# Optimization experiments

Measured on AMD Instinct MI355X. Metric: run time of the kernel, lower is better.

Reference implementation:

```python
import math
import jax, jax.numpy as jnp
import numpy as np

N_HEADS = 8
WINDOW = 4


def _get_relative_embeddings(emb, length, window):
    # emb: [1, 2*window+1, k_channels] -> [1, 2*length-1, k_channels]
    pad_length = max(length - (window + 1), 0)
    start = max(window + 1 - length, 0)
    if pad_length > 0:
        emb = jnp.pad(emb, ((0, 0), (pad_length, pad_length), (0, 0)))
    return emb[:, start:start + 2 * length - 1]


def _relative_position_to_absolute_position(x):
    # x: [b, h, l, 2l-1] -> [b, h, l, l] (skewing trick)
    b, h, l, _ = x.shape
    x = jnp.pad(x, ((0, 0), (0, 0), (0, 0), (0, 1)))
    x_flat = x.reshape(b, h, l * 2 * l)
    x_flat = jnp.pad(x_flat, ((0, 0), (0, 0), (0, l - 1)))
    return x_flat.reshape(b, h, l + 1, 2 * l - 1)[:, :, :l, l - 1:]


def _absolute_position_to_relative_position(x):
    # x: [b, h, l, l] -> [b, h, l, 2l-1]
    b, h, l, _ = x.shape
    x = jnp.pad(x, ((0, 0), (0, 0), (0, 0), (0, l - 1)))
    x_flat = x.reshape(b, h, l * l + l * (l - 1))
    x_flat = jnp.pad(x_flat, ((0, 0), (0, 0), (l, 0)))
    return x_flat.reshape(b, h, l, 2 * l)[:, :, :, 1:]


def setup_inputs() -> dict:
    key = jax.random.key(0)
    ks = jax.random.split(key, 12)
    b, t, d = 4, 1024, 512
    kc = d // N_HEADS
    s = 1.0 / math.sqrt(d)
    return {
        "x": jax.random.normal(ks[0], (b, t, d), jnp.float32),
        "c": jax.random.normal(ks[1], (b, t, d), jnp.float32),
        "wq": jax.random.normal(ks[2], (d, d), jnp.float32) * s,
        "bq": jnp.zeros((d,), jnp.float32),
        "wk": jax.random.normal(ks[3], (d, d), jnp.float32) * s,
        "bk": jnp.zeros((d,), jnp.float32),
        "wv": jax.random.normal(ks[4], (d, d), jnp.float32) * s,
        "bv": jnp.zeros((d,), jnp.float32),
        "wo": jax.random.normal(ks[5], (d, d), jnp.float32) * s,
        "bo": jnp.zeros((d,), jnp.float32),
        "emb_rel_k": jax.random.normal(ks[6], (1, 2 * WINDOW + 1, kc), jnp.float32) * kc ** -0.5,
        "emb_rel_v": jax.random.normal(ks[7], (1, 2 * WINDOW + 1, kc), jnp.float32) * kc ** -0.5,
    }


def reference(x, c, wq, bq, wk, bk, wv, bv, wo, bo, emb_rel_k, emb_rel_v):
    b, t, d = x.shape
    h = N_HEADS
    kc = d // h
    inv_sqrt = 1.0 / math.sqrt(kc)

    # 1x1 conv projections (pointwise matmul)
    q = x @ wq + bq   # [b, t, d]
    k = c @ wk + bk
    v = c @ wv + bv

    # Faithful reshape as in source: [b, t, d] -> [b, h, kc, t] -> [b, h, t, kc]
    q = q.reshape(b, h, kc, t).transpose(0, 1, 3, 2)
    k = k.reshape(b, h, kc, t).transpose(0, 1, 3, 2)
    v = v.reshape(b, h, kc, t).transpose(0, 1, 3, 2)

    scores = jnp.einsum('bhtd,bhsd->bhts', q, k) * inv_sqrt  # [b,h,t,t]

    # relative key logits
    key_rel = _get_relative_embeddings(emb_rel_k, t, WINDOW)[0]  # [2t-1, kc]
    rel_logits = jnp.einsum('bhtd,md->bhtm', q, key_rel)          # [b,h,t,2t-1]
    scores_local = _relative_position_to_absolute_position(rel_logits) * inv_sqrt
    scores = scores + scores_local

    p_attn = jax.nn.softmax(scores, axis=-1)
    output = jnp.einsum('bhts,bhsd->bhtd', p_attn, v)  # [b,h,t,kc]

    # relative value contribution
    rel_weights = _absolute_position_to_relative_position(p_attn)  # [b,h,t,2t-1]
    val_rel = _get_relative_embeddings(emb_rel_v, t, WINDOW)[0]    # [2t-1, kc]
    output = output + jnp.einsum('bhtm,md->bhtd', rel_weights, val_rel)

    # Faithful output reshape: [b,h,t,kc] -> [b,h,kc,t] -> [b,t,d]
    output = output.transpose(0, 1, 3, 2).reshape(b, t, d)
    out = output @ wo + bo
    return out
```

## Files before the change

### kernel.cpp

```cpp
#include <hip/hip_runtime.h>
#include <hip/hip_bf16.h>

#define NB 4
#define NT 1024
#define ND 512
#define NH 8
#define NKC 64

typedef __bf16 bf16x8 __attribute__((ext_vector_type(8)));
typedef float f32x4 __attribute__((ext_vector_type(4)));

__device__ __forceinline__ f32x4 MFMA(bf16x8 a, bf16x8 b, f32x4 c) {
    return __builtin_amdgcn_mfma_f32_16x16x32_bf16(a, b, c, 0, 0, 0);
}
__device__ __forceinline__ unsigned short f2bu(float v) {
    __hip_bfloat16 b = __float2bfloat16(v);
    return *(unsigned short*)&b;
}
__device__ __forceinline__ void split1(float v, unsigned short& h, unsigned short& l)
{
    __hip_bfloat16 hb = __float2bfloat16(v);
    float r = v - __bfloat162float(hb);
    __hip_bfloat16 lb = __float2bfloat16(r);
    h = *(unsigned short*)&hb;
    l = *(unsigned short*)&lb;
}
__device__ __forceinline__ void splitpack(const float4 a, const float4 b, uint4& h, uint4& l)
{
    union { unsigned short u[8]; uint4 v; } H, L;
    const float f[8] = {a.x, a.y, a.z, a.w, b.x, b.y, b.z, b.w};
    #pragma unroll
    for (int j = 0; j < 8; ++j) split1(f[j], H.u[j], L.u[j]);
    h = H.v; l = L.v;
}

__global__ __launch_bounds__(256)
void splitT_kernel(const float* __restrict__ w0, const float* __restrict__ w1,
                   const float* __restrict__ w2, const float* __restrict__ w3,
                   unsigned short* __restrict__ wT)
{
    __shared__ float tl[32][33];
    const float* w = (blockIdx.z == 0) ? w0 : (blockIdx.z == 1) ? w1
                   : (blockIdx.z == 2) ? w2 : w3;
    unsigned short* hi = wT + (size_t)blockIdx.z * 2 * (ND * ND);
    unsigned short* lo = hi + ND * ND;
    const int t = threadIdx.x;
    const int x0 = blockIdx.x * 32, y0 = blockIdx.y * 32;
    {
        const int r = t >> 3, c = (t & 7) * 4;
        const float4 v = *(const float4*)&w[(size_t)(y0 + r) * ND + x0 + c];
        tl[r][c] = v.x; tl[r][c+1] = v.y; tl[r][c+2] = v.z; tl[r][c+3] = v.w;
    }
    __syncthreads();
    {
        const int nr = t >> 3, k4 = (t & 7) * 4;
        unsigned short hh[4], ll[4];
        #pragma unroll
        for (int j = 0; j < 4; ++j) split1(tl[k4 + j][nr], hh[j], ll[j]);
        ushort4 h = make_ushort4(hh[0], hh[1], hh[2], hh[3]);
        ushort4 l = make_ushort4(ll[0], ll[1], ll[2], ll[3]);
        *(ushort4*)&hi[(size_t)(x0 + nr) * ND + y0 + k4] = h;
        *(ushort4*)&lo[(size_t)(x0 + nr) * ND + y0 + k4] = l;
    }
}

__global__ __launch_bounds__(256, 3)
void proj_mfma(const float* __restrict__ x, const float* __restrict__ cc,
               const unsigned short* __restrict__ wT,
               const float* __restrict__ bq, const float* __restrict__ bk,
               const float* __restrict__ bv,
               unsigned short* __restrict__ qh_o, unsigned short* __restrict__ ql_o,
               unsigned short* __restrict__ kh_o, unsigned short* __restrict__ vh_o)
{
    __shared__ unsigned short smem[12288];
    unsigned short* Ah = smem;
    unsigned short* Al = smem + 2048;
    unsigned short* Bh = smem + 4096;
    unsigned short* Bl = smem + 8192;
    unsigned short* Tr = smem;

    const int which = blockIdx.z;
    const float* A_g = (which == 0) ? x : cc;
    const unsigned short* Bh_g = wT + (size_t)which * 2 * (ND * ND);
    const unsigned short* Bl_g = Bh_g + ND * ND;
    const float* bias = (which == 0) ? bq : (which == 1) ? bk : bv;

    const int tid = threadIdx.x, l = tid & 63, w = tid >> 6;
    const int quad = l >> 4, lc = l & 15;
    const int wm = w & 1, wn = w >> 1;
    const int n0 = blockIdx.x * 128, m0 = blockIdx.y * 64;

    const int am = tid >> 2, ak = (tid & 3) * 8;
    const size_t aG = (size_t)(m0 + am) * ND + ak;
    const int bn = tid >> 1, bk2 = (tid & 1) * 16;
    const size_t bG = (size_t)(n0 + bn) * ND + bk2;

    float4 ra0 = *(const float4*)&A_g[aG];
    float4 ra1 = *(const float4*)&A_g[aG + 4];
    uint4 rb0 = *(const uint4*)&Bh_g[bG];
    uint4 rb1 = *(const uint4*)&Bh_g[bG + 8];
    uint4 rb2 = {}, rb3 = {};
    if (which != 2) {
        rb2 = *(const uint4*)&Bl_g[bG];
        rb3 = *(const uint4*)&Bl_g[bG + 8];
    }
    uint4 sh0, sl0;
    splitpack(ra0, ra1, sh0, sl0);

    f32x4 acc[2][4];
    #pragma unroll
    for (int mi = 0; mi < 2; ++mi)
        #pragma unroll
        for (int ni = 0; ni < 4; ++ni) acc[mi][ni] = (f32x4){0.f, 0.f, 0.f, 0.f};

    for (int k0 = 0; k0 < ND; k0 += 32) {
        __syncthreads();
        {
            *(uint4*)&Ah[am * 32 + ak] = sh0;
            *(uint4*)&Al[am * 32 + ak] = sl0;
            *(uint4*)&Bh[bn * 32 + bk2] = rb0; *(uint4*)&Bh[bn * 32 + bk2 + 8] = rb1;
            if (which != 2) {
                *(uint4*)&Bl[bn * 32 + bk2] = rb2; *(uint4*)&Bl[bn * 32 + bk2 + 8] = rb3;
            }
        }
        __syncthreads();
        const bool hasNext = (k0 + 32 < ND);
        if (hasNext) {
            const size_t aN = aG + k0 + 32, bN = bG + k0 + 32;
            ra0 = *(const float4*)&A_g[aN];
            ra1 = *(const float4*)&A_g[aN + 4];
            rb0 = *(const uint4*)&Bh_g[bN];
            rb1 = *(const uint4*)&Bh_g[bN + 8];
            if (which != 2) {
                rb2 = *(const uint4*)&Bl_g[bN];
                rb3 = *(const uint4*)&Bl_g[bN + 8];
            }
        }

        bf16x8 ah[2], al2[2], bh[4], bl[4];
        #pragma unroll
        for (int mi = 0; mi < 2; ++mi) {
            const int ar = (wm * 32 + mi * 16 + lc) * 32 + quad * 8;
            ah[mi] = *(const bf16x8*)&Ah[ar];
            al2[mi] = *(const bf16x8*)&Al[ar];
        }
        #pragma unroll
        for (int ni = 0; ni < 4; ++ni) {
            const int br = (wn * 64 + ni * 16 + lc) * 32 + quad * 8;
            bh[ni] = *(const bf16x8*)&Bh[br];
            if (which != 2) bl[ni] = *(const bf16x8*)&Bl[br];
        }
        if (which != 2) {
            #pragma unroll
            for (int mi = 0; mi < 2; ++mi)
                #pragma unroll
                for (int ni = 0; ni < 4; ++ni) {
                    acc[mi][ni] = MFMA(al2[mi], bh[ni], acc[mi][ni]);
                    acc[mi][ni] = MFMA(ah[mi], bl[ni], acc[mi][ni]);
                    acc[mi][ni] = MFMA(ah[mi], bh[ni], acc[mi][ni]);
                }
        } else {
            #pragma unroll
            for (int mi = 0; mi < 2; ++mi)
                #pragma unroll
                for (int ni = 0; ni < 4; ++ni) {
                    acc[mi][ni] = MFMA(al2[mi], bh[ni], acc[mi][ni]);
                    acc[mi][ni] = MFMA(ah[mi], bh[ni], acc[mi][ni]);
                }
        }
        if (hasNext) splitpack(ra0, ra1, sh0, sl0);
    }

    const int bb = m0 >> 10, tt0 = m0 & 1023;
    const int hh = tt0 >> 7, cch0 = (tt0 & 127) >> 1;
    const int bh_idx = bb * NH + hh;

    if (which == 2) {
        #pragma unroll
        for (int ni = 0; ni < 4; ++ni) {
            const int n = n0 + wn * 64 + ni * 16 + lc;
            const float bval = bias[n];
            #pragma unroll
            for (int mi = 0; mi < 2; ++mi)
                #pragma unroll
                for (int r = 0; r < 4; ++r) {
                    const int mloc = wm * 32 + mi * 16 + quad * 4 + r;
                    const int cch = cch0 + (mloc >> 1);
                    const int t = (mloc & 1) * 512 + n;
                    vh_o[(((size_t)bh_idx * 16 + (t >> 6)) * 64 + cch) * 64 + (t & 63)] =
                        f2bu(acc[mi][ni][r] + bval);
                }
        }
        return;
    }

    const int npass = (which == 0) ? 2 : 1;
    unsigned short* outp[2] = {(which == 0) ? qh_o : kh_o, ql_o};

    for (int pass = 0; pass < npass; ++pass) {
        __syncthreads();
        #pragma unroll
        for (int ni = 0; ni < 4; ++ni) {
            const int nloc = wn * 64 + ni * 16 + lc;
            const float bval = bias[n0 + nloc];
            #pragma unroll
            for (int mi = 0; mi < 2; ++mi)
                #pragma unroll
                for (int r = 0; r < 4; ++r) {
                    const int mloc = wm * 32 + mi * 16 + quad * 4 + r;
                    const float val = acc[mi][ni][r] + bval;
                    unsigned short hs, ls;
                    if (which == 0) { split1(val, hs, ls); }
                    else { hs = f2bu(val); ls = 0; }
                    Tr[((mloc & 1) * 128 + nloc) * 40 + (mloc >> 1)] =
                        (pass == 0) ? hs : ls;
                }
        }
        __syncthreads();
        {
            const int t = (tid >> 7) * 512 + n0 + (tid & 127);
            const size_t oa = ((size_t)bh_idx * NT + t) * NKC + cch0;
            const uint4 v0 = *(const uint4*)&Tr[tid * 40];
            const uint4 v1 = *(const uint4*)&Tr[tid * 40 + 8];
            const uint4 v2 = *(const uint4*)&Tr[tid * 40 + 16];
            const uint4 v3 = *(const uint4*)&Tr[tid * 40 + 24];
            *(uint4*)&outp[pass][oa]      = v0;
            *(uint4*)&outp[pass][oa + 8]  = v1;
            *(uint4*)&outp[pass][oa + 16] = v2;
            *(uint4*)&outp[pass][oa + 24] = v3;
        }
    }
}

__global__ __launch_bounds__(256, 4)
void attn_mfma(const unsigned short* __restrict__ qh_g, const unsigned short* __restrict__ ql_g,
               const unsigned short* __restrict__ kh_g,
               const unsigned short* __restrict__ vh_g,
               const float* __restrict__ embk, const float* __restrict__ embv,
               float* __restrict__ O0, float* __restrict__ O1,
               float* __restrict__ l0_g, float* __restrict__ l1_g)
{
    __shared__ unsigned short smem[19456];
    unsigned short* KsH = smem;
    unsigned short* Vt  = smem + 4608;
    unsigned short* Ps  = smem + 11264;
    float* bandv = (float*)(smem + 17920);
    unsigned short* EkH = smem + 11264;

    const int tid = threadIdx.x, l = tid & 63, w = tid >> 6;
    const int quad = l >> 4, lc = l & 15;
    const int q0 = (blockIdx.x >> 1) * 64;
    const int sh = blockIdx.x & 1;
    const int sBeg = sh * 512;
    const int hh = blockIdx.y, bb = blockIdx.z;
    const int bh = bb * NH + hh;
    const size_t qkBase = (size_t)bh * NT * NKC;
    const size_t vtBase = (size_t)bh * (16 * 64 * 64);
    float* Op = sh ? O1 : O0;
    float* lp = sh ? l1_g : l0_g;

    const int srow = tid >> 2, sseg = (tid & 3) * 16;

    auto loadKV = [&](uint4& k0r, uint4& k1r, uint4& v0r, uint4& v1r, int tile) {
        const size_t ka = qkBase + (size_t)(sBeg + tile * 64 + srow) * NKC + sseg;
        const size_t va = vtBase + (size_t)((sBeg >> 6) + tile) * 4096 + srow * 64 + sseg;
        k0r = *(const uint4*)&kh_g[ka];
        k1r = *(const uint4*)&kh_g[ka + 8];
        v0r = *(const uint4*)&vh_g[va];
        v1r = *(const uint4*)&vh_g[va + 8];
    };

    uint4 ak0, ak1, av0, av1, bk0, bk1, bv0, bv1;
    loadKV(ak0, ak1, av0, av1, 0);
    loadKV(bk0, bk1, bv0, bv1, 1);

    for (int idx = tid; idx < 16 * 72; idx += 256) {
        const int d = idx / 72, kc = idx - d * 72;
        EkH[idx] = f2bu((d < 9 && kc < 64) ? embk[d * 64 + kc] : 0.f);
    }
    for (int idx = tid; idx < 64 * 40; idx += 256) {
        const int c = idx / 40, col = 64 + (idx - c * 40);
        const int d = col - 64;
        Vt[c * 104 + col] = f2bu((d < 9) ? embv[d * 64 + c] : 0.f);
    }
    __syncthreads();

    bf16x8 qh[2], ql[2];
    {
        const int qg = q0 + w * 16 + lc;
        const size_t qa = qkBase + (size_t)qg * NKC + quad * 8;
        qh[0] = *(const bf16x8*)&qh_g[qa];
        qh[1] = *(const bf16x8*)&qh_g[qa + 32];
        ql[0] = *(const bf16x8*)&ql_g[qa];
        ql[1] = *(const bf16x8*)&ql_g[qa + 32];
    }

    {
        f32x4 accB = (f32x4){0.f, 0.f, 0.f, 0.f};
        #pragma unroll
        for (int kk = 0; kk < 2; ++kk) {
            const bf16x8 ebh = *(const bf16x8*)&EkH[lc * 72 + kk * 32 + quad * 8];
            accB = MFMA(ql[kk], ebh, accB);
            accB = MFMA(qh[kk], ebh, accB);
        }
        __syncthreads();
        if (lc <= 8) {
            #pragma unroll
            for (int r = 0; r < 4; ++r)
                bandv[(w * 16 + quad * 4 + r) * 12 + lc] = accB[r];
        }
    }
    unsigned short* P = Ps + w * 1664;
    {
        const int zr = l >> 2, zc = 80 + (l & 3) * 4;
        *(ushort4*)&P[zr * 104 + zc] = make_ushort4(0, 0, 0, 0);
    }

    f32x4 O[4];
    #pragma unroll
    for (int ci = 0; ci < 4; ++ci) O[ci] = (f32x4){0.f, 0.f, 0.f, 0.f};
    float l_run[4] = {0.f, 0.f, 0.f, 0.f};

    auto tilestep = [&](uint4& k0r, uint4& k1r, uint4& v0r, uint4& v1r,
                        int i, int nextTile) {
        const int s0 = sBeg + i * 64;
        __syncthreads();
        *(uint4*)&KsH[srow * 72 + sseg]      = k0r;
        *(uint4*)&KsH[srow * 72 + sseg + 8]  = k1r;
        *(uint4*)&Vt[srow * 104 + sseg]      = v0r;
        *(uint4*)&Vt[srow * 104 + sseg + 8]  = v1r;
        __syncthreads();
        if (nextTile >= 0) loadKV(k0r, k1r, v0r, v1r, nextTile);

        f32x4 S[4];
        #pragma unroll
        for (int ni = 0; ni < 4; ++ni) {
            f32x4 a = (f32x4){0.f, 0.f, 0.f, 0.f};
            #pragma unroll
            for (int kk = 0; kk < 2; ++kk) {
                const bf16x8 kb = *(const bf16x8*)&KsH[(ni * 16 + lc) * 72 + kk * 32 + quad * 8];
                a = MFMA(ql[kk], kb, a);
                a = MFMA(qh[kk], kb, a);
            }
            S[ni] = a;
        }

        #pragma unroll
        for (int ni = 0; ni < 4; ++ni)
            #pragma unroll
            for (int r = 0; r < 4; ++r) {
                const int ql64 = w * 16 + quad * 4 + r;
                const int dp4 = (s0 + ni * 16 + lc) - (q0 + ql64) + 4;
                float sv = S[ni][r];
                if (dp4 >= 0 && dp4 <= 8) sv += bandv[ql64 * 12 + dp4];
                S[ni][r] = __expf(sv * 0.125f);
            }
        #pragma unroll
        for (int r = 0; r < 4; ++r)
            l_run[r] += S[0][r] + S[1][r] + S[2][r] + S[3][r];

        {
            const int zr = l >> 2, zc = 64 + (l & 3) * 4;
            *(ushort4*)&P[zr * 104 + zc] = make_ushort4(0, 0, 0, 0);
        }
        #pragma unroll
        for (int ni = 0; ni < 4; ++ni)
            #pragma unroll
            for (int r = 0; r < 4; ++r) {
                const int prow = quad * 4 + r;
                const unsigned short pb = f2bu(S[ni][r]);
                P[prow * 104 + ni * 16 + lc] = pb;
                const int dp4 = (s0 + ni * 16 + lc) - (q0 + w * 16 + prow) + 4;
                if (dp4 >= 0 && dp4 <= 8) P[prow * 104 + 64 + dp4] = pb;
            }

        #pragma unroll
        for (int ks = 0; ks < 3; ++ks) {
            const bf16x8 pa = *(const bf16x8*)&P[lc * 104 + ks * 32 + quad * 8];
            #pragma unroll
            for (int ci = 0; ci < 4; ++ci) {
                const bf16x8 vb = *(const bf16x8*)&Vt[(ci * 16 + lc) * 104 + ks * 32 + quad * 8];
                O[ci] = MFMA(pa, vb, O[ci]);
            }
        }
    };

    for (int ii = 0; ii < 8; ii += 2) {
        tilestep(ak0, ak1, av0, av1, ii,     (ii + 2 < 8) ? ii + 2 : -1);
        tilestep(bk0, bk1, bv0, bv1, ii + 1, (ii + 3 < 8) ? ii + 3 : -1);
    }

    #pragma unroll
    for (int r = 0; r < 4; ++r) {
        float v = l_run[r];
        v += __shfl_xor(v, 1); v += __shfl_xor(v, 2);
        v += __shfl_xor(v, 4); v += __shfl_xor(v, 8);
        l_run[r] = v;
    }
    const int qg0 = q0 + w * 16 + quad * 4;
    if (lc == 0) {
        #pragma unroll
        for (int r = 0; r < 4; ++r)
            lp[(size_t)bh * NT + qg0 + r] = l_run[r];
    }
    float* Os = (float*)smem;
    __syncthreads();
    #pragma unroll
    for (int ci = 0; ci < 4; ++ci)
        #pragma unroll
        for (int r = 0; r < 4; ++r)
            Os[(ci * 16 + lc) * 68 + w * 16 + quad * 4 + r] = O[ci][r];
    __syncthreads();
    {
        const int c = tid >> 2, q4 = (tid & 3) * 16;
        const size_t ob = ((size_t)bh * 64 + c) * NT + q0 + q4;
        #pragma unroll
        for (int i4 = 0; i4 < 16; i4 += 4)
            *(f32x4*)&Op[ob + i4] = *(const f32x4*)&Os[c * 68 + q4 + i4];
    }
}

__global__ __launch_bounds__(256)
void combine_kernel(const float* __restrict__ O0, const float* __restrict__ O1,
                    const float* __restrict__ l0_g, const float* __restrict__ l1_g,
                    unsigned short* __restrict__ ath)
{
    const int q0 = blockIdx.x * 64, hh = blockIdx.y, bb = blockIdx.z;
    const int bh = bb * NH + hh;
    const int tid = threadIdx.x;
    __shared__ float linv[64];
    if (tid < 64)
        linv[tid] = 1.f / (l0_g[(size_t)bh * NT + q0 + tid] +
                           l1_g[(size_t)bh * NT + q0 + tid]);
    __syncthreads();

    const int c = tid >> 2, qq = (tid & 3) * 16;
    const size_t ib = ((size_t)bh * 64 + c) * NT + q0 + qq;
    union { unsigned short u[16]; uint4 v[2]; } out;
    #pragma unroll
    for (int j = 0; j < 16; j += 4) {
        const f32x4 a = *(const f32x4*)&O0[ib + j];
        const f32x4 b = *(const f32x4*)&O1[ib + j];
        #pragma unroll
        for (int r = 0; r < 4; ++r)
            out.u[j + r] = f2bu((a[r] + b[r]) * linv[qq + j + r]);
    }
    const int row = hh * 128 + 2 * c + (q0 >> 9);
    const size_t oa = ((size_t)bb * NT + row) * ND + (q0 & 511) + qq;
    *(uint4*)&ath[oa]     = out.v[0];
    *(uint4*)&ath[oa + 8] = out.v[1];
}

__global__ __launch_bounds__(256, 4)
void outproj_mfma(const unsigned short* __restrict__ a_g,
                  const unsigned short* __restrict__ wTh,
                  const float* __restrict__ bo, float* __restrict__ out)
{
    __shared__ unsigned short As[64 * 32], Bh[64 * 32], Bl[64 * 32];
    const unsigned short* Bl_g = wTh + ND * ND;
    const int tid = threadIdx.x, l = tid & 63, w = tid >> 6;
    const int quad = l >> 4, lc = l & 15;
    const int wm = w & 1, wn = w >> 1;
    const int n0 = blockIdx.x * 64, m0 = blockIdx.y * 64;

    const int sm = tid >> 2, sk = (tid & 3) * 8;
    const size_t aG = (size_t)(m0 + sm) * ND + sk;
    const size_t bG = (size_t)(n0 + sm) * ND + sk;

    uint4 ra  = *(const uint4*)&a_g[aG];
    uint4 rbh = *(const uint4*)&wTh[bG];
    uint4 rbl = *(const uint4*)&Bl_g[bG];

    f32x4 acc[2][2];
    #pragma unroll
    for (int mi = 0; mi < 2; ++mi)
        #pragma unroll
        for (int ni = 0; ni < 2; ++ni) acc[mi][ni] = (f32x4){0.f, 0.f, 0.f, 0.f};

    for (int k0 = 0; k0 < ND; k0 += 32) {
        __syncthreads();
        *(uint4*)&As[sm * 32 + sk] = ra;
        *(uint4*)&Bh[sm * 32 + sk] = rbh;
        *(uint4*)&Bl[sm * 32 + sk] = rbl;
        __syncthreads();
        if (k0 + 32 < ND) {
            ra  = *(const uint4*)&a_g[aG + k0 + 32];
            rbh = *(const uint4*)&wTh[bG + k0 + 32];
            rbl = *(const uint4*)&Bl_g[bG + k0 + 32];
        }
        bf16x8 ab[2], bhf[2], blf[2];
        #pragma unroll
        for (int mi = 0; mi < 2; ++mi)
            ab[mi] = *(const bf16x8*)&As[(wm * 32 + mi * 16 + lc) * 32 + quad * 8];
        #pragma unroll
        for (int ni = 0; ni < 2; ++ni) {
            const int br = (wn * 32 + ni * 16 + lc) * 32 + quad * 8;
            bhf[ni] = *(const bf16x8*)&Bh[br];
            blf[ni] = *(const bf16x8*)&Bl[br];
        }
        #pragma unroll
        for (int mi = 0; mi < 2; ++mi)
            #pragma unroll
            for (int ni = 0; ni < 2; ++ni) {
                acc[mi][ni] = MFMA(ab[mi], bhf[ni], acc[mi][ni]);
                acc[mi][ni] = MFMA(ab[mi], blf[ni], acc[mi][ni]);
            }
    }

    #pragma unroll
    for (int ni = 0; ni < 2; ++ni) {
        const int n = n0 + wn * 32 + ni * 16 + lc;
        const float bval = bo[n];
        #pragma unroll
        for (int mi = 0; mi < 2; ++mi)
            #pragma unroll
            for (int r = 0; r < 4; ++r) {
                const int m = m0 + wm * 32 + mi * 16 + quad * 4 + r;
                out[(size_t)m * ND + n] = acc[mi][ni][r] + bval;
            }
    }
}

extern "C" void kernel_launch(void* const* d_in, const int* in_sizes, int n_in,
                              void* d_out, int out_size, void* d_ws, size_t ws_size,
                              hipStream_t stream) {
    const float* x    = (const float*)d_in[0];
    const float* c    = (const float*)d_in[1];
    const float* wq   = (const float*)d_in[2];
    const float* bq   = (const float*)d_in[3];
    const float* wk   = (const float*)d_in[4];
    const float* bk   = (const float*)d_in[5];
    const float* wv   = (const float*)d_in[6];
    const float* bv   = (const float*)d_in[7];
    const float* wo   = (const float*)d_in[8];
    const float* bo   = (const float*)d_in[9];
    const float* embk = (const float*)d_in[10];
    const float* embv = (const float*)d_in[11];

    unsigned short* u16 = (unsigned short*)d_ws;
    const size_t M = 1024 * 1024;
    unsigned short* wT  = u16;
    unsigned short* qh  = u16 + 2 * M;
    unsigned short* ql  = u16 + 4 * M;
    unsigned short* kh  = u16 + 6 * M;
    unsigned short* vh  = u16 + 8 * M;
    unsigned short* ath = u16 + 10 * M;
    float* fbase = (float*)(u16 + 12 * M);
    float* O0   = fbase;
    float* O1   = fbase + 2 * M;
    float* l0_g = fbase + 4 * M;
    float* l1_g = l0_g + 32768;

    splitT_kernel<<<dim3(16, 16, 4), 256, 0, stream>>>(wq, wk, wv, wo, wT);

    proj_mfma<<<dim3(4, 64, 3), 256, 0, stream>>>(x, c, wT, bq, bk, bv,
                                                  qh, ql, kh, vh);

    attn_mfma<<<dim3(32, 8, 4), 256, 0, stream>>>(qh, ql, kh, vh,
                                                  embk, embv, O0, O1, l0_g, l1_g);

    combine_kernel<<<dim3(16, 8, 4), 256, 0, stream>>>(O0, O1, l0_g, l1_g, ath);

    outproj_mfma<<<dim3(8, 64), 256, 0, stream>>>(ath,
                                                  wT + (size_t)3 * 2 * ND * ND,
                                                  bo, (float*)d_out);
}
```

Baseline: 171.2 us.

## Read K/V MFMA operands directly from global memory, drop LDS staging and barriers

The attention kernel stops staging K and V tiles through shared memory with register prefetch and block barriers. Each wave now loads its MFMA operands straight from global memory (through the caches), and the relative-value embedding gets its own small LDS array. The output transpose through LDS is replaced by direct strided f32x4 stores. This removes barriers and LDS traffic and cuts LDS use, which may raise occupancy. In exchange, each of the four waves reloads the same K/V data from global/L2 with less coalesced access and no explicit prefetch, so memory latency may be exposed.

New measurement: 193.0 us. 1.13x slower.

```diff
diff --git a/kernel.cpp b/kernel.cpp
--- a/kernel.cpp
+++ b/kernel.cpp
@@ -240,12 +240,10 @@
                float* __restrict__ O0, float* __restrict__ O1,
                float* __restrict__ l0_g, float* __restrict__ l1_g)
 {
-    __shared__ unsigned short smem[19456];
-    unsigned short* KsH = smem;
-    unsigned short* Vt  = smem + 4608;
-    unsigned short* Ps  = smem + 11264;
-    float* bandv = (float*)(smem + 17920);
-    unsigned short* EkH = smem + 11264;
+    __shared__ float bandv[64 * 12];
+    __shared__ unsigned short EvT[64 * 40];
+    __shared__ unsigned short EkH[16 * 72];
+    __shared__ unsigned short Ps[4 * 16 * 104];
 
     const int tid = threadIdx.x, l = tid & 63, w = tid >> 6;
     const int quad = l >> 4, lc = l & 15;
@@ -259,29 +257,18 @@
     float* Op = sh ? O1 : O0;
     float* lp = sh ? l1_g : l0_g;
 
-    const int srow = tid >> 2, sseg = (tid & 3) * 16;
-
-    auto loadKV = [&](uint4& k0r, uint4& k1r, uint4& v0r, uint4& v1r, int tile) {
-        const size_t ka = qkBase + (size_t)(sBeg + tile * 64 + srow) * NKC + sseg;
-        const size_t va = vtBase + (size_t)((sBeg >> 6) + tile) * 4096 + srow * 64 + sseg;
-        k0r = *(const uint4*)&kh_g[ka];
-        k1r = *(const uint4*)&kh_g[ka + 8];
-        v0r = *(const uint4*)&vh_g[va];
-        v1r = *(const uint4*)&vh_g[va + 8];
-    };
-
-    uint4 ak0, ak1, av0, av1, bk0, bk1, bv0, bv1;
-    loadKV(ak0, ak1, av0, av1, 0);
-    loadKV(bk0, bk1, bv0, bv1, 1);
-
     for (int idx = tid; idx < 16 * 72; idx += 256) {
         const int d = idx / 72, kc = idx - d * 72;
         EkH[idx] = f2bu((d < 9 && kc < 64) ? embk[d * 64 + kc] : 0.f);
     }
     for (int idx = tid; idx < 64 * 40; idx += 256) {
-        const int c = idx / 40, col = 64 + (idx - c * 40);
-        const int d = col - 64;
-        Vt[c * 104 + col] = f2bu((d < 9) ? embv[d * 64 + c] : 0.f);
+        const int c = idx / 40, d = idx - c * 40;
+        EvT[idx] = f2bu((d < 9) ? embv[d * 64 + c] : 0.f);
+    }
+    unsigned short* P = Ps + w * 1664;
+    {
+        const int zr = l >> 2, zc = 80 + (l & 3) * 4;
+        *(ushort4*)&P[zr * 104 + zc] = make_ushort4(0, 0, 0, 0);
     }
     __syncthreads();
 
@@ -303,34 +290,22 @@
             accB = MFMA(ql[kk], ebh, accB);
             accB = MFMA(qh[kk], ebh, accB);
         }
-        __syncthreads();
         if (lc <= 8) {
             #pragma unroll
             for (int r = 0; r < 4; ++r)
                 bandv[(w * 16 + quad * 4 + r) * 12 + lc] = accB[r];
         }
     }
-    unsigned short* P = Ps + w * 1664;
-    {
-        const int zr = l >> 2, zc = 80 + (l & 3) * 4;
-        *(ushort4*)&P[zr * 104 + zc] = make_ushort4(0, 0, 0, 0);
-    }
 
     f32x4 O[4];
     #pragma unroll
     for (int ci = 0; ci < 4; ++ci) O[ci] = (f32x4){0.f, 0.f, 0.f, 0.f};
     float l_run[4] = {0.f, 0.f, 0.f, 0.f};
 
-    auto tilestep = [&](uint4& k0r, uint4& k1r, uint4& v0r, uint4& v1r,
-                        int i, int nextTile) {
+    for (int i = 0; i < 8; ++i) {
         const int s0 = sBeg + i * 64;
-        __syncthreads();
-        *(uint4*)&KsH[srow * 72 + sseg]      = k0r;
-        *(uint4*)&KsH[srow * 72 + sseg + 8]  = k1r;
-        *(uint4*)&Vt[srow * 104 + sseg]      = v0r;
-        *(uint4*)&Vt[srow * 104 + sseg + 8]  = v1r;
-        __syncthreads();
-        if (nextTile >= 0) loadKV(k0r, k1r, v0r, v1r, nextTile);
+        const size_t kRow = qkBase + (size_t)s0 * NKC;
+        const size_t vTile = vtBase + (size_t)((sBeg >> 6) + i) * 4096;
 
         f32x4 S[4];
         #pragma unroll
@@ -338,7 +313,8 @@
             f32x4 a = (f32x4){0.f, 0.f, 0.f, 0.f};
             #pragma unroll
             for (int kk = 0; kk < 2; ++kk) {
-                const bf16x8 kb = *(const bf16x8*)&KsH[(ni * 16 + lc) * 72 + kk * 32 + quad * 8];
+                const bf16x8 kb = *(const bf16x8*)&kh_g[kRow +
+                    (size_t)(ni * 16 + lc) * NKC + kk * 32 + quad * 8];
                 a = MFMA(ql[kk], kb, a);
                 a = MFMA(qh[kk], kb, a);
             }
@@ -375,19 +351,23 @@
             }
 
         #pragma unroll
-        for (int ks = 0; ks < 3; ++ks) {
+        for (int ks = 0; ks < 2; ++ks) {
             const bf16x8 pa = *(const bf16x8*)&P[lc * 104 + ks * 32 + quad * 8];
             #pragma unroll
             for (int ci = 0; ci < 4; ++ci) {
-                const bf16x8 vb = *(const bf16x8*)&Vt[(ci * 16 + lc) * 104 + ks * 32 + quad * 8];
+                const bf16x8 vb = *(const bf16x8*)&vh_g[vTile +
+                    (size_t)(ci * 16 + lc) * 64 + ks * 32 + quad * 8];
                 O[ci] = MFMA(pa, vb, O[ci]);
             }
         }
-    };
-
-    for (int ii = 0; ii < 8; ii += 2) {
-        tilestep(ak0, ak1, av0, av1, ii,     (ii + 2 < 8) ? ii + 2 : -1);
-        tilestep(bk0, bk1, bv0, bv1, ii + 1, (ii + 3 < 8) ? ii + 3 : -1);
+        {
+            const bf16x8 pa2 = *(const bf16x8*)&P[lc * 104 + 64 + quad * 8];
+            #pragma unroll
+            for (int ci = 0; ci < 4; ++ci) {
+                const bf16x8 vb = *(const bf16x8*)&EvT[(ci * 16 + lc) * 40 + quad * 8];
+                O[ci] = MFMA(pa2, vb, O[ci]);
+            }
+        }
     }
 
     #pragma unroll
@@ -403,20 +383,10 @@
         for (int r = 0; r < 4; ++r)
             lp[(size_t)bh * NT + qg0 + r] = l_run[r];
     }
-    float* Os = (float*)smem;
-    __syncthreads();
-    #pragma unroll
-    for (int ci = 0; ci < 4; ++ci)
-        #pragma unroll
-        for (int r = 0; r < 4; ++r)
-            Os[(ci * 16 + lc) * 68 + w * 16 + quad * 4 + r] = O[ci][r];
-    __syncthreads();
-    {
-        const int c = tid >> 2, q4 = (tid & 3) * 16;
-        const size_t ob = ((size_t)bh * 64 + c) * NT + q0 + q4;
-        #pragma unroll
-        for (int i4 = 0; i4 < 16; i4 += 4)
-            *(f32x4*)&Op[ob + i4] = *(const f32x4*)&Os[c * 68 + q4 + i4];
+    #pragma unroll
+    for (int ci = 0; ci < 4; ++ci) {
+        const int c = ci * 16 + lc;
+        *(f32x4*)&Op[((size_t)bh * 64 + c) * NT + qg0] = O[ci];
     }
 }
 
```
